# Optimization experiments

Measured on AMD Instinct MI355X. Metric: run time of the kernel, lower is better.

## Reference

```python
import jax, jax.numpy as jnp
import numpy as np

NEG_SLOPE = 0.2
NUM_GRAPHS = 512


def gat_conv(x, W, att_src, att_dst, bias, src, dst, n):
    """Single-head PyG GATConv (concat=True trivially, heads=1).
    x: [N, Fin], W: [Fin, Fout], att_*: [Fout], bias: [Fout].
    src/dst: [E] int32/64 (self-loops already appended).
    """
    h = x @ W                               # [N, Fout]
    a_s = h @ att_src                       # [N]
    a_d = h @ att_dst                       # [N]
    e = a_s[src] + a_d[dst]                 # [E]
    e = jnp.where(e >= 0, e, NEG_SLOPE * e)  # LeakyReLU
    # numerically stable edge-softmax grouped by destination node
    m = jax.ops.segment_max(e, dst, num_segments=n)          # [N]
    w = jnp.exp(e - m[dst])                                   # [E]
    denom = jax.ops.segment_sum(w, dst, num_segments=n)      # [N]
    alpha = w / denom[dst]                                    # [E]
    out = jax.ops.segment_sum(alpha[:, None] * h[src], dst, num_segments=n)
    return out + bias


def setup_inputs() -> dict:
    key = jax.random.key(0)
    ks = jax.random.split(key, 12)
    N, E, FIN, H = 50000, 800000, 768, 64
    x = jax.random.normal(ks[0], (N, FIN), dtype=jnp.float32)
    edge_index = jax.random.randint(ks[1], (2, E), 0, N, dtype=jnp.int64)
    batch = jnp.sort(jax.random.randint(ks[2], (N,), 0, NUM_GRAPHS, dtype=jnp.int64))
    def glorot(k, shape):
        lim = np.sqrt(6.0 / (shape[0] + shape[-1]))
        return jax.random.uniform(k, shape, jnp.float32, -lim, lim)
    return {
        "x": x, "edge_index": edge_index, "batch": batch,
        "W1": glorot(ks[3], (FIN, H)),
        "att_src1": glorot(ks[4], (H,)), "att_dst1": glorot(ks[5], (H,)),
        "b1": jnp.zeros((H,), jnp.float32),
        "W2": glorot(ks[6], (H, H)),
        "att_src2": glorot(ks[7], (H,)), "att_dst2": glorot(ks[8], (H,)),
        "b2": jnp.zeros((H,), jnp.float32),
        "Wlin": glorot(ks[9], (H, 2)),
        "blin": jnp.zeros((2,), jnp.float32),
    }


def reference(x, edge_index, batch, W1, att_src1, att_dst1, b1,
              W2, att_src2, att_dst2, b2, Wlin, blin):
    n = x.shape[0]
    loops = jnp.arange(n, dtype=edge_index.dtype)
    src = jnp.concatenate([edge_index[0], loops])  # add_self_loops=True
    dst = jnp.concatenate([edge_index[1], loops])
    h = gat_conv(x, W1, att_src1, att_dst1, b1, src, dst, n)
    h = jax.nn.relu(h)
    h = gat_conv(h, W2, att_src2, att_dst2, b2, src, dst, n)
    h = jax.nn.relu(h)
    # global_mean_pool
    sums = jax.ops.segment_sum(h, batch, num_segments=NUM_GRAPHS)     # [G, H]
    cnt = jax.ops.segment_sum(jnp.ones((n,), h.dtype), batch, num_segments=NUM_GRAPHS)
    pooled = sums / jnp.maximum(cnt, 1.0)[:, None]
    return pooled @ Wlin + blin
```

## Files before the change

kernel.cpp:

```cpp
#include <hip/hip_runtime.h>

#define NEG_SLOPE 0.2f
#define NGRAPHS 512

typedef short short8 __attribute__((ext_vector_type(8)));
typedef float f32x4 __attribute__((ext_vector_type(4)));

__device__ __forceinline__ float wave_reduce_sum(float v) {
#pragma unroll
    for (int off = 32; off > 0; off >>= 1) v += __shfl_xor(v, off, 64);
    return v;
}
__device__ __forceinline__ float wave_reduce_max(float v) {
#pragma unroll
    for (int off = 32; off > 0; off >>= 1) v = fmaxf(v, __shfl_xor(v, off, 64));
    return v;
}
__device__ __forceinline__ unsigned short f2bf(float f) {
    unsigned u = __float_as_uint(f);
    u += 0x7FFFu + ((u >> 16) & 1u);
    return (unsigned short)(u >> 16);
}

__device__ __forceinline__ void edge_sd(const int* __restrict__ ei, int E, int e,
                                        int& s, int& d) {
    if (e < E) { s = ei[e]; d = ei[E + e]; }
    else { s = d = e - E; }
}

__global__ __launch_bounds__(256) void setup_hist(
    const int* __restrict__ ei, int E, int ET, int* __restrict__ counts,
    int nEdgeBlk, const float* __restrict__ W1, unsigned short* __restrict__ Wt1,
    int K1, const float* __restrict__ W2, unsigned short* __restrict__ Wt2,
    const int* __restrict__ batch, int* __restrict__ gstart, int N) {
    const int b = blockIdx.x, tid = threadIdx.x;
    if (b < nEdgeBlk) {
        int e = b * 256 + tid;
        if (e >= ET) return;
        int s, d;
        edge_sd(ei, E, e, s, d);
        atomicAdd(counts + d, 1);
    } else if (b < nEdgeBlk + 64) {
        int n = b - nEdgeBlk;
        for (int k = tid; k < K1; k += 256)
            Wt1[(size_t)n * K1 + k] = f2bf(W1[(size_t)k * 64 + n]);
    } else if (b == nEdgeBlk + 64) {
#pragma unroll
        for (int i = 0; i < 16; ++i) {
            int idx = tid + i * 256;
            int n = idx >> 6, k = idx & 63;
            Wt2[n * 64 + k] = f2bf(W2[k * 64 + n]);
        }
    } else {
        for (int g = tid; g <= NGRAPHS; g += 256) {
            int lo = 0, hi = N;
            while (lo < hi) {
                int mid = (lo + hi) >> 1;
                if (batch[mid] < g) lo = mid + 1; else hi = mid;
            }
            gstart[g] = lo;
        }
    }
}

__global__ __launch_bounds__(256) void scan_sum(const int* __restrict__ counts,
                                                int* __restrict__ blk_sum, int N,
                                                int CH) {
    __shared__ int wsum[4];
    const int tid = threadIdx.x, lane = tid & 63, wid = tid >> 6;
    const int b = blockIdx.x;
    int begin = b * CH, endi = min(begin + CH, N);
    int s = 0;
    for (int i = begin + tid; i < endi; i += 256) s += counts[i];
#pragma unroll
    for (int off = 32; off > 0; off >>= 1) s += __shfl_xor(s, off, 64);
    if (lane == 0) wsum[wid] = s;
    __syncthreads();
    if (tid == 0) blk_sum[b] = wsum[0] + wsum[1] + wsum[2] + wsum[3];
}

__global__ __launch_bounds__(64) void scan_blk(int* __restrict__ blk_sum,
                                               int* __restrict__ row_ptr, int N,
                                               int nb) {
    int t = threadIdx.x;
    int v = (t < nb) ? blk_sum[t] : 0;
    int sv = v;
#pragma unroll
    for (int off = 1; off < 64; off <<= 1) {
        int u = __shfl_up(sv, off, 64);
        if (t >= off) sv += u;
    }
    if (t < nb) blk_sum[t] = sv - v;
    if (t == nb - 1) row_ptr[N] = sv;
}

__global__ __launch_bounds__(256) void scan_local(const int* __restrict__ counts,
                                                  const int* __restrict__ blk_off,
                                                  int* __restrict__ row_ptr,
                                                  int* __restrict__ next_, int N,
                                                  int CH) {
    __shared__ int wsum[4];
    __shared__ int ctot;
    const int tid = threadIdx.x, lane = tid & 63, wid = tid >> 6;
    const int b = blockIdx.x;
    int begin = b * CH, endi = min(begin + CH, N);
    int carry = blk_off[b];
    for (int base = begin; base < endi; base += 256) {
        int i = base + tid;
        int v = (i < endi) ? counts[i] : 0;
        int sv = v;
#pragma unroll
        for (int off = 1; off < 64; off <<= 1) {
            int u = __shfl_up(sv, off, 64);
            if (lane >= off) sv += u;
        }
        if (lane == 63) wsum[wid] = sv;
        __syncthreads();
        if (tid == 0) {
            int a = 0;
#pragma unroll
            for (int j = 0; j < 4; ++j) { int u = wsum[j]; wsum[j] = a; a += u; }
            ctot = a;
        }
        __syncthreads();
        int excl = carry + wsum[wid] + sv - v;
        if (i < endi) { row_ptr[i] = excl; next_[i] = excl; }
        carry += ctot;
        __syncthreads();
    }
}

__global__ __launch_bounds__(256, 4) void gemm1_fill(
    const float* __restrict__ A, const unsigned short* __restrict__ Wt, int M, int K,
    float* __restrict__ h, const float* __restrict__ att_s,
    const float* __restrict__ att_d, float* __restrict__ a_s,
    float* __restrict__ a_d, int nGemm, const int* __restrict__ ei, int E, int ET,
    int* __restrict__ next_, int* __restrict__ srcs) {
    const int tid = threadIdx.x;
    if (blockIdx.x >= nGemm) {
        int e = (blockIdx.x - nGemm) * 256 + tid;
        if (e >= ET) return;
        int s, d;
        edge_sd(ei, E, e, s, d);
        int pos = atomicAdd(next_ + d, 1);
        srcs[pos] = s;
        return;
    }
    const int w = tid >> 6, l = tid & 63, m = l & 15, q = l >> 4;
    const int row0 = blockIdx.x * 64;
    const int r = row0 + w * 16 + m;
    const bool rok = r < M;
    const float* Ap = A + (size_t)r * K + q * 8;
    const unsigned short* Bp = Wt + (size_t)m * K + q * 8;
    f32x4 acc0 = {0.f, 0.f, 0.f, 0.f}, acc1 = acc0, acc2 = acc0, acc3 = acc0;
#pragma unroll 8
    for (int t = 0; t < 24; ++t) {
        short8 av = {0, 0, 0, 0, 0, 0, 0, 0};
        if (rok) {
            const float4 f0 = *(const float4*)(Ap + t * 32);
            const float4 f1 = *(const float4*)(Ap + t * 32 + 4);
            unsigned short tt[8] = {f2bf(f0.x), f2bf(f0.y), f2bf(f0.z), f2bf(f0.w),
                                    f2bf(f1.x), f2bf(f1.y), f2bf(f1.z), f2bf(f1.w)};
            av = *(const short8*)tt;
        }
        const unsigned short* bp = Bp + t * 32;
        acc0 = __builtin_amdgcn_mfma_f32_16x16x32_bf16(
            av, *(const short8*)(bp), acc0, 0, 0, 0);
        acc1 = __builtin_amdgcn_mfma_f32_16x16x32_bf16(
            av, *(const short8*)(bp + (size_t)16 * K), acc1, 0, 0, 0);
        acc2 = __builtin_amdgcn_mfma_f32_16x16x32_bf16(
            av, *(const short8*)(bp + (size_t)32 * K), acc2, 0, 0, 0);
        acc3 = __builtin_amdgcn_mfma_f32_16x16x32_bf16(
            av, *(const short8*)(bp + (size_t)48 * K), acc3, 0, 0, 0);
    }
    float as0 = att_s[m], as1 = att_s[16 + m], as2 = att_s[32 + m], as3 = att_s[48 + m];
    float ad0 = att_d[m], ad1 = att_d[16 + m], ad2 = att_d[32 + m], ad3 = att_d[48 + m];
    const int rowb = row0 + w * 16 + q * 4;
#pragma unroll
    for (int rr = 0; rr < 4; ++rr) {
        int row = rowb + rr;
        float v0 = acc0[rr], v1 = acc1[rr], v2 = acc2[rr], v3 = acc3[rr];
        if (row < M) {
            float* hp = h + (size_t)row * 64 + m;
            hp[0] = v0; hp[16] = v1; hp[32] = v2; hp[48] = v3;
        }
        float hs = v0 * as0 + v1 * as1 + v2 * as2 + v3 * as3;
        float hd = v0 * ad0 + v1 * ad1 + v2 * ad2 + v3 * ad3;
#pragma unroll
        for (int off = 1; off < 16; off <<= 1) {
            hs += __shfl_xor(hs, off, 64);
            hd += __shfl_xor(hd, off, 64);
        }
        if (m == 0 && row < M) { a_s[row] = hs; a_d[row] = hd; }
    }
}

__global__ __launch_bounds__(256) void gemm2_mfma(
    const unsigned short* __restrict__ Ab, const unsigned short* __restrict__ Wt2,
    int M, float* __restrict__ h, const float* __restrict__ att_s,
    const float* __restrict__ att_d, float* __restrict__ a_s,
    float* __restrict__ a_d) {
    const int tid = threadIdx.x;
    const int w = tid >> 6, l = tid & 63, m = l & 15, q = l >> 4;
    const int row0 = blockIdx.x * 64;
    const int r = row0 + w * 16 + m;
    short8 av0 = {0, 0, 0, 0, 0, 0, 0, 0}, av1 = av0;
    if (r < M) {
        av0 = *(const short8*)(Ab + (size_t)r * 64 + q * 8);
        av1 = *(const short8*)(Ab + (size_t)r * 64 + 32 + q * 8);
    }
    f32x4 acc0 = {0.f, 0.f, 0.f, 0.f}, acc1 = acc0, acc2 = acc0, acc3 = acc0;
    const unsigned short* bp = Wt2 + (size_t)m * 64 + q * 8;
    acc0 = __builtin_amdgcn_mfma_f32_16x16x32_bf16(av0, *(const short8*)(bp), acc0, 0, 0, 0);
    acc0 = __builtin_amdgcn_mfma_f32_16x16x32_bf16(av1, *(const short8*)(bp + 32), acc0, 0, 0, 0);
    acc1 = __builtin_amdgcn_mfma_f32_16x16x32_bf16(av0, *(const short8*)(bp + 16 * 64), acc1, 0, 0, 0);
    acc1 = __builtin_amdgcn_mfma_f32_16x16x32_bf16(av1, *(const short8*)(bp + 16 * 64 + 32), acc1, 0, 0, 0);
    acc2 = __builtin_amdgcn_mfma_f32_16x16x32_bf16(av0, *(const short8*)(bp + 32 * 64), acc2, 0, 0, 0);
    acc2 = __builtin_amdgcn_mfma_f32_16x16x32_bf16(av1, *(const short8*)(bp + 32 * 64 + 32), acc2, 0, 0, 0);
    acc3 = __builtin_amdgcn_mfma_f32_16x16x32_bf16(av0, *(const short8*)(bp + 48 * 64), acc3, 0, 0, 0);
    acc3 = __builtin_amdgcn_mfma_f32_16x16x32_bf16(av1, *(const short8*)(bp + 48 * 64 + 32), acc3, 0, 0, 0);

    float as0 = att_s[m], as1 = att_s[16 + m], as2 = att_s[32 + m], as3 = att_s[48 + m];
    float ad0 = att_d[m], ad1 = att_d[16 + m], ad2 = att_d[32 + m], ad3 = att_d[48 + m];
    const int rowb = row0 + w * 16 + q * 4;
#pragma unroll
    for (int rr = 0; rr < 4; ++rr) {
        int row = rowb + rr;
        float v0 = acc0[rr], v1 = acc1[rr], v2 = acc2[rr], v3 = acc3[rr];
        if (row < M) {
            float* hp = h + (size_t)row * 64 + m;
            hp[0] = v0; hp[16] = v1; hp[32] = v2; hp[48] = v3;
        }
        float hs = v0 * as0 + v1 * as1 + v2 * as2 + v3 * as3;
        float hd = v0 * ad0 + v1 * ad1 + v2 * ad2 + v3 * ad3;
#pragma unroll
        for (int off = 1; off < 16; off <<= 1) {
            hs += __shfl_xor(hs, off, 64);
            hd += __shfl_xor(hd, off, 64);
        }
        if (m == 0 && row < M) { a_s[row] = hs; a_d[row] = hd; }
    }
}

__global__ __launch_bounds__(256) void gat_agg_kernel(
    const int* __restrict__ row_ptr, const int* __restrict__ srcs,
    const float* __restrict__ a_s, const float* __restrict__ a_d,
    const float* __restrict__ h, const float* __restrict__ bias,
    float* __restrict__ out, unsigned short* __restrict__ outb, int N) {
    int n = blockIdx.x * 4 + (threadIdx.x >> 6);
    int lane = threadIdx.x & 63;
    if (n >= N) return;
    const int start = row_ptr[n];
    const int deg = row_ptr[n + 1] - start;
    const float adn = a_d[n];

    if (deg <= 64) {
        int sl = 0;
        float v = -1e30f;
        if (lane < deg) {
            sl = srcs[start + lane];
            float t = a_s[sl] + adn;
            v = (t >= 0.f) ? t : NEG_SLOPE * t;
        }
        float m = wave_reduce_max(v);
        float wl = (lane < deg) ? __expf(v - m) : 0.f;
        float l = wave_reduce_sum(wl);
        wl *= (1.f / l);

        const int eq = lane >> 4, fq = lane & 15;
        float ax = 0.f, ay = 0.f, az = 0.f, aw = 0.f;
        for (int j = 0; j < deg; j += 4) {
            int idx = j + eq;
            bool ok = idx < deg;
            int ii = ok ? idx : 0;
            float a = __shfl(wl, ii, 64);
            int s = __shfl(sl, ii, 64);
            if (!ok) a = 0.f;
            const float4 hv = *(const float4*)(h + (size_t)s * 64 + fq * 4);
            ax += a * hv.x; ay += a * hv.y; az += a * hv.z; aw += a * hv.w;
        }
#pragma unroll
        for (int off = 16; off <= 32; off <<= 1) {
            ax += __shfl_xor(ax, off, 64);
            ay += __shfl_xor(ay, off, 64);
            az += __shfl_xor(az, off, 64);
            aw += __shfl_xor(aw, off, 64);
        }
        if (eq == 0) {
            const float4 bv = *(const float4*)(bias + fq * 4);
            float4 o;
            o.x = ax + bv.x; o.y = ay + bv.y; o.z = az + bv.z; o.w = aw + bv.w;
            o.x = o.x > 0.f ? o.x : 0.f;
            o.y = o.y > 0.f ? o.y : 0.f;
            o.z = o.z > 0.f ? o.z : 0.f;
            o.w = o.w > 0.f ? o.w : 0.f;
            if (out) *(float4*)(out + (size_t)n * 64 + fq * 4) = o;
            if (outb) {
                unsigned short t[4] = {f2bf(o.x), f2bf(o.y), f2bf(o.z), f2bf(o.w)};
                *(uint2*)(outb + (size_t)n * 64 + fq * 4) = *(uint2*)t;
            }
        }
        return;
    }

    const int end = start + deg;
    float m = -1e30f;
    for (int i = start + lane; i < end; i += 64) {
        float v = a_s[srcs[i]] + adn;
        v = (v >= 0.f) ? v : NEG_SLOPE * v;
        m = fmaxf(m, v);
    }
    m = wave_reduce_max(m);
    float l = 0.f;
    for (int i = start + lane; i < end; i += 64) {
        float v = a_s[srcs[i]] + adn;
        v = (v >= 0.f) ? v : NEG_SLOPE * v;
        l += __expf(v - m);
    }
    l = wave_reduce_sum(l);
    const float inv_den = 1.f / l;
    float acc = 0.f;
    for (int c = start; c < end; c += 64) {
        int cl = end - c;
        if (cl > 64) cl = 64;
        int sl = 0;
        float wl = 0.f;
        if (c + lane < end) {
            sl = srcs[c + lane];
            float v = a_s[sl] + adn;
            v = (v >= 0.f) ? v : NEG_SLOPE * v;
            wl = __expf(v - m) * inv_den;
        }
        for (int j = 0; j < cl; ++j) {
            float wj = __shfl(wl, j, 64);
            int sj = __shfl(sl, j, 64);
            acc += wj * h[(size_t)sj * 64 + lane];
        }
    }
    float o = acc + bias[lane];
    o = o > 0.f ? o : 0.f;
    if (out) out[(size_t)n * 64 + lane] = o;
    if (outb) outb[(size_t)n * 64 + lane] = f2bf(o);
}

__global__ __launch_bounds__(256) void pool_final(const float* __restrict__ x,
                                                  const int* __restrict__ gstart,
                                                  const float* __restrict__ Wlin,
                                                  const float* __restrict__ blin,
                                                  float* __restrict__ out) {
    __shared__ float red[4][64];
    const int g = blockIdx.x;
    const int lane = threadIdx.x & 63, w = threadIdx.x >> 6;
    const int s = gstart[g], e = gstart[g + 1];
    float acc = 0.f;
    for (int n = s + w; n < e; n += 4) acc += x[(size_t)n * 64 + lane];
    red[w][lane] = acc;
    __syncthreads();
    if (w == 0) {
        float p = red[0][lane] + red[1][lane] + red[2][lane] + red[3][lane];
        int c = e - s;
        p /= (float)(c > 1 ? c : 1);
        float o0 = wave_reduce_sum(p * Wlin[lane * 2 + 0]);
        float o1 = wave_reduce_sum(p * Wlin[lane * 2 + 1]);
        if (lane == 0) {
            out[g * 2 + 0] = o0 + blin[0];
            out[g * 2 + 1] = o1 + blin[1];
        }
    }
}

extern "C" void kernel_launch(void* const* d_in, const int* in_sizes, int n_in,
                              void* d_out, int out_size, void* d_ws, size_t ws_size,
                              hipStream_t stream) {
    const float* x    = (const float*)d_in[0];
    const int*   ei   = (const int*)d_in[1];
    const int*   batch= (const int*)d_in[2];
    const float* W1   = (const float*)d_in[3];
    const float* as1  = (const float*)d_in[4];
    const float* ad1  = (const float*)d_in[5];
    const float* b1   = (const float*)d_in[6];
    const float* W2   = (const float*)d_in[7];
    const float* as2  = (const float*)d_in[8];
    const float* ad2  = (const float*)d_in[9];
    const float* b2   = (const float*)d_in[10];
    const float* Wlin = (const float*)d_in[11];
    const float* blin = (const float*)d_in[12];
    float* out = (float*)d_out;

    const int FIN = 768;
    const int N  = in_sizes[0] / FIN;
    const int E  = in_sizes[1] / 2;
    const int ET = E + N;
    const size_t N64 = (size_t)N * 64;
    const int NB = 64;
    const int CH = (N + NB - 1) / NB;

    float* ws     = (float*)d_ws;
    float* hbuf   = ws;
    float* x2     = hbuf + N64;
    float* a_s    = x2 + N64;
    float* a_d    = a_s + N;
    int* counts   = (int*)(a_d + N);
    int* row_ptr  = counts + N;
    int* next     = row_ptr + N + 1;
    int* blk_sum  = next + N;
    int* gstart   = blk_sum + 64;
    int* srcs     = gstart + NGRAPHS + 1;
    uintptr_t wtp = (uintptr_t)(srcs + ET);
    wtp = (wtp + 15) & ~(uintptr_t)15;
    unsigned short* Wt1 = (unsigned short*)wtp;
    unsigned short* Wt2 = Wt1 + (size_t)64 * FIN;
    unsigned short* x1b = Wt2 + (size_t)64 * 64;

    const int nEdgeBlk  = (ET + 255) / 256;
    const int nWaveBlkN = (N + 3) / 4;
    const int nGemmBlk  = (N + 63) / 64;

    hipMemsetAsync(counts, 0, (size_t)N * sizeof(int), stream);

    setup_hist<<<nEdgeBlk + 66, 256, 0, stream>>>(ei, E, ET, counts, nEdgeBlk,
                                                  W1, Wt1, FIN, W2, Wt2,
                                                  batch, gstart, N);
    scan_sum<<<NB, 256, 0, stream>>>(counts, blk_sum, N, CH);
    scan_blk<<<1, 64, 0, stream>>>(blk_sum, row_ptr, N, NB);
    scan_local<<<NB, 256, 0, stream>>>(counts, blk_sum, row_ptr, next, N, CH);

    gemm1_fill<<<nGemmBlk + nEdgeBlk, 256, 0, stream>>>(
        x, Wt1, N, FIN, hbuf, as1, ad1, a_s, a_d, nGemmBlk, ei, E, ET, next, srcs);
    gat_agg_kernel<<<nWaveBlkN, 256, 0, stream>>>(row_ptr, srcs, a_s, a_d, hbuf,
                                                  b1, nullptr, x1b, N);

    gemm2_mfma<<<nGemmBlk, 256, 0, stream>>>(x1b, Wt2, N, hbuf, as2, ad2, a_s, a_d);
    gat_agg_kernel<<<nWaveBlkN, 256, 0, stream>>>(row_ptr, srcs, a_s, a_d, hbuf,
                                                  b2, x2, nullptr, N);

    pool_final<<<NGRAPHS, 256, 0, stream>>>(x2, gstart, Wlin, blin, out);
}
```

Measured before the change: 459.2 us.

## Record per-edge rank during histogram and fill CSR without atomics in separate kernel

The histogram pass now stores each edge's atomic slot rank, so CSR construction becomes an atomic-free scatter (row_ptr[d]+rank[e]) in its own kernel, removing the next_ array and the second atomic pass. The fill is split out of the GEMM1 launch, and GEMM1 drops its row-validity branch by clamping the row index and fully unrolling the K loop. This costs an extra launch, an extra ET-sized rank write and read, and lost overlap between the fill and the GEMM.

```diff
diff --git a/kernel.cpp b/kernel.cpp
--- a/kernel.cpp
+++ b/kernel.cpp
@@ -32,14 +32,15 @@
     const int* __restrict__ ei, int E, int ET, int* __restrict__ counts,
     int nEdgeBlk, const float* __restrict__ W1, unsigned short* __restrict__ Wt1,
     int K1, const float* __restrict__ W2, unsigned short* __restrict__ Wt2,
-    const int* __restrict__ batch, int* __restrict__ gstart, int N) {
+    const int* __restrict__ batch, int* __restrict__ gstart, int N,
+    int* __restrict__ rank) {
     const int b = blockIdx.x, tid = threadIdx.x;
     if (b < nEdgeBlk) {
         int e = b * 256 + tid;
         if (e >= ET) return;
         int s, d;
         edge_sd(ei, E, e, s, d);
-        atomicAdd(counts + d, 1);
+        rank[e] = atomicAdd(counts + d, 1);
     } else if (b < nEdgeBlk + 64) {
         int n = b - nEdgeBlk;
         for (int k = tid; k < K1; k += 256)
@@ -96,8 +97,7 @@
 
 __global__ __launch_bounds__(256) void scan_local(const int* __restrict__ counts,
                                                   const int* __restrict__ blk_off,
-                                                  int* __restrict__ row_ptr,
-                                                  int* __restrict__ next_, int N,
+                                                  int* __restrict__ row_ptr, int N,
                                                   int CH) {
     __shared__ int wsum[4];
     __shared__ int ctot;
@@ -124,45 +124,44 @@
         }
         __syncthreads();
         int excl = carry + wsum[wid] + sv - v;
-        if (i < endi) { row_ptr[i] = excl; next_[i] = excl; }
+        if (i < endi) row_ptr[i] = excl;
         carry += ctot;
         __syncthreads();
     }
 }
 
-__global__ __launch_bounds__(256, 4) void gemm1_fill(
-    const float* __restrict__ A, const unsigned short* __restrict__ Wt, int M, int K,
-    float* __restrict__ h, const float* __restrict__ att_s,
+__global__ __launch_bounds__(256) void fill_csr(const int* __restrict__ ei, int E,
+                                                int ET,
+                                                const int* __restrict__ row_ptr,
+                                                const int* __restrict__ rank,
+                                                int* __restrict__ srcs) {
+    int e = blockIdx.x * 256 + threadIdx.x;
+    if (e >= ET) return;
+    int s, d;
+    edge_sd(ei, E, e, s, d);
+    srcs[row_ptr[d] + rank[e]] = s;
+}
+
+__global__ __launch_bounds__(256, 4) void gemm1_mfma(
+    const float* __restrict__ A, const unsigned short* __restrict__ Wt, int M,
+    int K, float* __restrict__ h, const float* __restrict__ att_s,
     const float* __restrict__ att_d, float* __restrict__ a_s,
-    float* __restrict__ a_d, int nGemm, const int* __restrict__ ei, int E, int ET,
-    int* __restrict__ next_, int* __restrict__ srcs) {
+    float* __restrict__ a_d) {
     const int tid = threadIdx.x;
-    if (blockIdx.x >= nGemm) {
-        int e = (blockIdx.x - nGemm) * 256 + tid;
-        if (e >= ET) return;
-        int s, d;
-        edge_sd(ei, E, e, s, d);
-        int pos = atomicAdd(next_ + d, 1);
-        srcs[pos] = s;
-        return;
-    }
     const int w = tid >> 6, l = tid & 63, m = l & 15, q = l >> 4;
     const int row0 = blockIdx.x * 64;
     const int r = row0 + w * 16 + m;
-    const bool rok = r < M;
-    const float* Ap = A + (size_t)r * K + q * 8;
+    const int rc = r < M ? r : M - 1;
+    const float4* Ap = (const float4*)(A + (size_t)rc * K) + q * 2;
     const unsigned short* Bp = Wt + (size_t)m * K + q * 8;
     f32x4 acc0 = {0.f, 0.f, 0.f, 0.f}, acc1 = acc0, acc2 = acc0, acc3 = acc0;
-#pragma unroll 8
+#pragma unroll
     for (int t = 0; t < 24; ++t) {
-        short8 av = {0, 0, 0, 0, 0, 0, 0, 0};
-        if (rok) {
-            const float4 f0 = *(const float4*)(Ap + t * 32);
-            const float4 f1 = *(const float4*)(Ap + t * 32 + 4);
-            unsigned short tt[8] = {f2bf(f0.x), f2bf(f0.y), f2bf(f0.z), f2bf(f0.w),
-                                    f2bf(f1.x), f2bf(f1.y), f2bf(f1.z), f2bf(f1.w)};
-            av = *(const short8*)tt;
-        }
+        const float4 f0 = Ap[t * 8];
+        const float4 f1 = Ap[t * 8 + 1];
+        unsigned short tt[8] = {f2bf(f0.x), f2bf(f0.y), f2bf(f0.z), f2bf(f0.w),
+                                f2bf(f1.x), f2bf(f1.y), f2bf(f1.z), f2bf(f1.w)};
+        short8 av = *(const short8*)tt;
         const unsigned short* bp = Bp + t * 32;
         acc0 = __builtin_amdgcn_mfma_f32_16x16x32_bf16(
             av, *(const short8*)(bp), acc0, 0, 0, 0);
@@ -402,11 +401,11 @@
     float* a_d    = a_s + N;
     int* counts   = (int*)(a_d + N);
     int* row_ptr  = counts + N;
-    int* next     = row_ptr + N + 1;
-    int* blk_sum  = next + N;
+    int* blk_sum  = row_ptr + N + 1;
     int* gstart   = blk_sum + 64;
     int* srcs     = gstart + NGRAPHS + 1;
-    uintptr_t wtp = (uintptr_t)(srcs + ET);
+    int* rank     = srcs + ET;
+    uintptr_t wtp = (uintptr_t)(rank + ET);
     wtp = (wtp + 15) & ~(uintptr_t)15;
     unsigned short* Wt1 = (unsigned short*)wtp;
     unsigned short* Wt2 = Wt1 + (size_t)64 * FIN;
@@ -420,13 +419,15 @@
 
     setup_hist<<<nEdgeBlk + 66, 256, 0, stream>>>(ei, E, ET, counts, nEdgeBlk,
                                                   W1, Wt1, FIN, W2, Wt2,
-                                                  batch, gstart, N);
+                                                  batch, gstart, N, rank);
     scan_sum<<<NB, 256, 0, stream>>>(counts, blk_sum, N, CH);
     scan_blk<<<1, 64, 0, stream>>>(blk_sum, row_ptr, N, NB);
-    scan_local<<<NB, 256, 0, stream>>>(counts, blk_sum, row_ptr, next, N, CH);
-
-    gemm1_fill<<<nGemmBlk + nEdgeBlk, 256, 0, stream>>>(
-        x, Wt1, N, FIN, hbuf, as1, ad1, a_s, a_d, nGemmBlk, ei, E, ET, next, srcs);
+    scan_local<<<NB, 256, 0, stream>>>(counts, blk_sum, row_ptr, N, CH);
+
+    fill_csr<<<nEdgeBlk, 256, 0, stream>>>(ei, E, ET, row_ptr, rank, srcs);
+
+    gemm1_mfma<<<nGemmBlk, 256, 0, stream>>>(x, Wt1, N, FIN, hbuf, as1, ad1,
+                                             a_s, a_d);
     gat_agg_kernel<<<nWaveBlkN, 256, 0, stream>>>(row_ptr, srcs, a_s, a_d, hbuf,
                                                   b1, nullptr, x1b, N);
 
```

Measured after the change: 458.7 us. No clear change (-0.1%).
